# Kernel tuning notes

Hardware: AMD Instinct MI355X
Metric: run time of the kernel (lower is better)

## Reference

```python
import jax, jax.numpy as jnp
import numpy as np

B, S, HID = 1, 2048, 2048
NUM_HEADS, NUM_KV_HEADS, HEAD_DIM = 16, 4, 128
ROPE_THETA = 10000.0
EPS = 1e-6


def setup_inputs() -> dict:
    key = jax.random.key(0)
    ks = jax.random.split(key, 9)
    s = 0.02
    return {
        "hidden_states": jax.random.normal(ks[0], (B, S, HID), jnp.float32),
        "mu_prev": jax.random.normal(ks[1], (B, S, HID), jnp.float32),
        "wq": jax.random.normal(ks[2], (NUM_HEADS * HEAD_DIM, HID), jnp.float32) * s,
        "wk": jax.random.normal(ks[3], (NUM_KV_HEADS * HEAD_DIM, HID), jnp.float32) * s,
        "wv": jax.random.normal(ks[4], (NUM_KV_HEADS * HEAD_DIM, HID), jnp.float32) * s,
        "wo": jax.random.normal(ks[5], (HID, NUM_HEADS * HEAD_DIM), jnp.float32) * s,
        "wmq": jax.random.normal(ks[6], (NUM_HEADS * HEAD_DIM, HID), jnp.float32) * (s * 0.1),
        "wmk": jax.random.normal(ks[7], (NUM_KV_HEADS * HEAD_DIM, HID), jnp.float32) * (s * 0.1),
        "wmv": jax.random.normal(ks[8], (NUM_KV_HEADS * HEAD_DIM, HID), jnp.float32) * (s * 0.1),
        "q_norm_w": jnp.ones((HEAD_DIM,), jnp.float32),
        "k_norm_w": jnp.ones((HEAD_DIM,), jnp.float32),
    }


def _rmsnorm(x, w):
    var = jnp.mean(jnp.square(x), axis=-1, keepdims=True)
    return x * jax.lax.rsqrt(var + EPS) * w


def _rope_cos_sin(seq_len, dtype):
    inv_freq = 1.0 / (ROPE_THETA ** (jnp.arange(0, HEAD_DIM, 2, dtype=jnp.float32) / HEAD_DIM))
    freqs = jnp.arange(seq_len, dtype=jnp.float32)[:, None] * inv_freq[None, :]  # [S, D/2]
    emb = jnp.concatenate([freqs, freqs], axis=-1)  # [S, D]
    return jnp.cos(emb).astype(dtype), jnp.sin(emb).astype(dtype)


def _rotate_half(x):
    x1, x2 = jnp.split(x, 2, axis=-1)
    return jnp.concatenate([-x2, x1], axis=-1)


def reference(hidden_states, mu_prev, wq, wk, wv, wo, wmq, wmk, wmv, q_norm_w, k_norm_w):
    b, s, _ = hidden_states.shape
    # Fused mu-guided QKV projections (cat(x, mu) @ cat(W, Wm)^T == x@W^T + mu@Wm^T)
    q = hidden_states @ wq.T + mu_prev @ wmq.T  # [B,S,H*D]
    k = hidden_states @ wk.T + mu_prev @ wmk.T  # [B,S,KV*D]
    v = hidden_states @ wv.T + mu_prev @ wmv.T
    q = q.reshape(b, s, NUM_HEADS, HEAD_DIM).transpose(0, 2, 1, 3)      # [B,H,S,D]
    k = k.reshape(b, s, NUM_KV_HEADS, HEAD_DIM).transpose(0, 2, 1, 3)   # [B,KV,S,D]
    v = v.reshape(b, s, NUM_KV_HEADS, HEAD_DIM).transpose(0, 2, 1, 3)
    # per-head QK RMSNorm
    q = _rmsnorm(q, q_norm_w)
    k = _rmsnorm(k, k_norm_w)
    # RoPE
    cos, sin = _rope_cos_sin(s, q.dtype)
    q = q * cos + _rotate_half(q) * sin
    k = k * cos + _rotate_half(k) * sin
    # GQA attention without materializing repeated K/V: group query heads
    g = NUM_HEADS // NUM_KV_HEADS
    qg = q.reshape(b, NUM_KV_HEADS, g, s, HEAD_DIM)
    scale = 1.0 / jnp.sqrt(jnp.asarray(HEAD_DIM, q.dtype))
    scores = jnp.einsum('bkgqd,bkld->bkgql', qg, k) * scale  # [B,KV,G,S,S]
    causal = jnp.tril(jnp.ones((s, s), bool))
    scores = jnp.where(causal, scores, jnp.asarray(-jnp.inf, scores.dtype))
    probs = jax.nn.softmax(scores.astype(jnp.float32), axis=-1).astype(q.dtype)
    out = jnp.einsum('bkgql,bkld->bkgqd', probs, v)  # [B,KV,G,S,D]
    out = out.reshape(b, NUM_HEADS, s, HEAD_DIM).transpose(0, 2, 1, 3).reshape(b, s, NUM_HEADS * HEAD_DIM)
    return out @ wo.T
```

## Files before the change

kernel.cpp:

```cpp
#include <hip/hip_runtime.h>
#include <math.h>

#define SEQ 2048
#define HID_DIM 2048
#define NH 16
#define NKV 4
#define HD 128
#define QS 3072

typedef float  f4v  __attribute__((ext_vector_type(4)));
typedef __bf16 bf8v __attribute__((ext_vector_type(8)));
typedef __bf16 bf4v __attribute__((ext_vector_type(4)));
typedef __bf16 bf2v __attribute__((ext_vector_type(2)));

typedef __attribute__((address_space(1))) const void* gvp;
typedef __attribute__((address_space(3))) void*       svp;

__device__ __forceinline__ void gld16(const void* g, void* lds_wave_base) {
    __builtin_amdgcn_global_load_lds((gvp)g, (svp)lds_wave_base, 16, 0, 0);
}

__device__ __forceinline__ void wgb() {
    asm volatile("" ::: "memory");
    __builtin_amdgcn_s_barrier();
    asm volatile("" ::: "memory");
}
#define VMC(n) asm volatile("s_waitcnt vmcnt(" #n ")" ::: "memory")

__global__ __launch_bounds__(256)
void cvt_all(__bf16* __restrict__ Acat, __bf16* __restrict__ Wcat,
             __bf16* __restrict__ Wo,
             const float* __restrict__ hs, const float* __restrict__ mu,
             const float* __restrict__ wq, const float* __restrict__ wmq,
             const float* __restrict__ wk, const float* __restrict__ wmk,
             const float* __restrict__ wv, const float* __restrict__ wmv,
             const float* __restrict__ wo)
{
    int b = blockIdx.x;
    const float *s0, *s1; __bf16* dst;
    if (b < 8192)       { s0 = hs; s1 = mu;  dst = Acat; }
    else if (b < 16384) { s0 = wq; s1 = wmq; dst = Wcat;                            b -= 8192; }
    else if (b < 18432) { s0 = wk; s1 = wmk; dst = Wcat + (size_t)2048 * 4096;      b -= 16384; }
    else if (b < 20480) { s0 = wv; s1 = wmv; dst = Wcat + (size_t)2560 * 4096;      b -= 18432; }
    else {
        int i = (b - 20480) * 256 + threadIdx.x;
        float4 v = *reinterpret_cast<const float4*>(wo + (size_t)i * 4);
        *reinterpret_cast<bf4v*>(Wo + (size_t)i * 4) =
            bf4v{ (__bf16)v.x, (__bf16)v.y, (__bf16)v.z, (__bf16)v.w };
        return;
    }
    int i = b * 256 + threadIdx.x;
    int row = i >> 10, c = i & 1023;
    const float* s = (c < 512) ? s0 + ((size_t)row * 512 + c) * 4
                               : s1 + ((size_t)row * 512 + (c - 512)) * 4;
    float4 v = *reinterpret_cast<const float4*>(s);
    *reinterpret_cast<bf4v*>(dst + ((size_t)row * 1024 + c) * 4) =
        bf4v{ (__bf16)v.x, (__bf16)v.y, (__bf16)v.z, (__bf16)v.w };
}

__device__ __forceinline__ void stage_half(
    const __bf16* __restrict__ g, int ldk, int row0, int ktile, int half,
    char* buf, int w, int sr, int sc)
{
#pragma unroll
    for (int j = 0; j < 2; ++j) {
        int sid = w * 2 + j;
        int rb = half * 8 + (sid >> 1), cb = sid & 1;
        gld16(g + (size_t)(row0 + rb * 16 + sr) * ldk + ktile * 64 + cb * 32 + sc,
              buf + (rb * 2 + cb) * 1024);
    }
}
__device__ __forceinline__ void stage_tile(
    const __bf16* __restrict__ g, int ldk, int row0, int ktile,
    char* buf, int w, int sr, int sc)
{
    stage_half(g, ldk, row0, ktile, 0, buf, w, sr, sc);
    stage_half(g, ldk, row0, ktile, 1, buf, w, sr, sc);
}

#define LOAD_AF(DST, BUF, MTB) \
    _Pragma("unroll") for (int mt = 0; mt < 4; ++mt) \
    _Pragma("unroll") for (int ks = 0; ks < 2; ++ks) \
        DST[mt][ks] = *(const bf8v*)((BUF) + (((wm * 8 + (MTB) + mt) * 2 + ks) << 10) + frag_off);
#define LOAD_BF(DST, BUF, NTB) \
    _Pragma("unroll") for (int nt = 0; nt < 2; ++nt) \
    _Pragma("unroll") for (int ks = 0; ks < 2; ++ks) \
        DST[nt][ks] = *(const bf8v*)((BUF) + (((wn * 4 + (NTB) + nt) * 2 + ks) << 10) + frag_off);
#define MFMA_Q(MTB, NTB, AR, BR) \
    __builtin_amdgcn_s_setprio(1); \
    _Pragma("unroll") for (int mt = 0; mt < 4; ++mt) \
    _Pragma("unroll") for (int nt = 0; nt < 2; ++nt) \
    _Pragma("unroll") for (int ks = 0; ks < 2; ++ks) \
        acc[(MTB) + mt][(NTB) + nt] = __builtin_amdgcn_mfma_f32_16x16x32_bf16( \
            AR[mt][ks], BR[nt][ks], acc[(MTB) + mt][(NTB) + nt], 0, 0, 0); \
    __builtin_amdgcn_s_setprio(0);

__global__ __launch_bounds__(512, 2)
void gemm_nt_pl(const __bf16* __restrict__ A, const __bf16* __restrict__ B,
                __bf16* __restrict__ P, int M, int N, int K, int KS)
{
    __shared__ __align__(1024) char lds[131072];
    char* A0 = lds;
    char* A1 = lds + 32768;
    char* B0 = lds + 65536;
    char* B1 = lds + 98304;

    const int tid = threadIdx.x, lane = tid & 63, w = tid >> 6;
    const int wm = w >> 2, wn = w & 3;
    const int mm = lane & 15, quad = lane >> 4;
    const int m0 = blockIdx.y * 256, n0 = blockIdx.x * 256;
    const int kt0 = (blockIdx.z * KS) >> 6;
    const int T = KS >> 6;

    const int sr = lane >> 2, sc = (lane & 3) * 8;
    const int frag_off = (mm * 4 + quad) << 4;

    f4v acc[8][4] = {};
    bf8v aLo[4][2], aHi[4][2], b01e[2][2], b01o[2][2], b23[2][2];

    stage_tile(A, K, m0, kt0,     A0, w, sr, sc);
    stage_tile(B, K, n0, kt0,     B0, w, sr, sc);
    stage_tile(A, K, m0, kt0 + 1, A1, w, sr, sc);
    stage_tile(B, K, n0, kt0 + 1, B1, w, sr, sc);
    VMC(8);
    wgb();
    LOAD_AF(aLo, A0, 0)
    LOAD_BF(b01e, B0, 0)

    const int nbody = (T - 2) >> 1;
    for (int it = 0; it < nbody; ++it) {
        const int t2 = kt0 + 2 * it + 2, t3 = t2 + 1;
        LOAD_BF(b23, B0, 2)
        MFMA_Q(0, 0, aLo, b01e)
        wgb();
        LOAD_AF(aHi, A0, 4)
        MFMA_Q(0, 2, aLo, b23)
        VMC(0);
        wgb();
        LOAD_AF(aLo, A1, 0)
        stage_tile(B, K, n0, t2, B0, w, sr, sc);
        MFMA_Q(4, 2, aHi, b23)
        wgb();
        LOAD_BF(b01o, B1, 0)
        stage_tile(A, K, m0, t2, A0, w, sr, sc);
        MFMA_Q(4, 0, aHi, b01e)
        wgb();
        LOAD_BF(b23, B1, 2)
        MFMA_Q(0, 0, aLo, b01o)
        wgb();
        LOAD_AF(aHi, A1, 4)
        MFMA_Q(0, 2, aLo, b23)
        VMC(0);
        wgb();
        LOAD_AF(aLo, A0, 0)
        stage_tile(B, K, n0, t3, B1, w, sr, sc);
        MFMA_Q(4, 2, aHi, b23)
        wgb();
        LOAD_BF(b01e, B0, 0)
        stage_tile(A, K, m0, t3, A1, w, sr, sc);
        MFMA_Q(4, 0, aHi, b01o)
        wgb();
    }
    LOAD_BF(b23, B0, 2)
    MFMA_Q(0, 0, aLo, b01e)
    wgb();
    LOAD_AF(aHi, A0, 4)
    MFMA_Q(0, 2, aLo, b23)
    VMC(0);
    wgb();
    LOAD_AF(aLo, A1, 0)
    MFMA_Q(4, 2, aHi, b23)
    wgb();
    LOAD_BF(b01o, B1, 0)
    MFMA_Q(4, 0, aHi, b01e)
    wgb();
    LOAD_BF(b23, B1, 2)
    MFMA_Q(0, 0, aLo, b01o)
    wgb();
    LOAD_AF(aHi, A1, 4)
    MFMA_Q(0, 2, aLo, b23)
    wgb();
    MFMA_Q(4, 2, aHi, b23)
    MFMA_Q(4, 0, aHi, b01o)

    __bf16* Pz = P + (size_t)blockIdx.z * M * N;
#pragma unroll
    for (int mt = 0; mt < 8; ++mt)
#pragma unroll
        for (int nt = 0; nt < 4; ++nt)
#pragma unroll
            for (int r = 0; r < 4; ++r)
                Pz[(size_t)(m0 + wm * 128 + mt * 16 + quad * 4 + r) * N
                   + n0 + wn * 64 + nt * 16 + mm] = (__bf16)acc[mt][nt][r];
}

__global__ __launch_bounds__(256)
void add4(const __bf16* __restrict__ P, float* __restrict__ out, int n4)
{
    int i = blockIdx.x * 256 + threadIdx.x;
    if (i >= n4) return;
    float4 s = {0.f, 0.f, 0.f, 0.f};
#pragma unroll
    for (int z = 0; z < 4; ++z) {
        bf4v v = *reinterpret_cast<const bf4v*>(P + (size_t)z * n4 * 4 + (size_t)i * 4);
        s.x += (float)v[0]; s.y += (float)v[1]; s.z += (float)v[2]; s.w += (float)v[3];
    }
    *reinterpret_cast<float4*>(out + (size_t)i * 4) = s;
}

__global__ __launch_bounds__(256)
void norm_rope_pk(__bf16* __restrict__ qkv ,
                  const __bf16* __restrict__ p1,
                  const float* __restrict__ qw, const float* __restrict__ kw,
                  __bf16* __restrict__ Kt)
{
    const int s = blockIdx.x, hh = blockIdx.y * 4 + threadIdx.y, l = threadIdx.x;
    const float* wn; float scale; int off;
    if (hh < NH) { off = hh * HD;               wn = qw; scale = 0.08838834764831845f; }
    else         { off = 2048 + (hh - NH) * HD; wn = kw; scale = 1.0f; }
    __bf16* p = qkv + (size_t)s * QS + off;
    const __bf16* q1 = p1 + (size_t)s * QS + off;
    float x0 = (float)p[l]      + (float)q1[l];
    float x1 = (float)p[l + 64] + (float)q1[l + 64];
    float ss = x0 * x0 + x1 * x1;
#pragma unroll
    for (int o = 32; o; o >>= 1) ss += __shfl_xor(ss, o);
    float inv = rsqrtf(ss * (1.0f / 128.0f) + 1e-6f);
    x0 *= inv * wn[l];
    x1 *= inv * wn[l + 64];
    float invf = exp2f(-(float)l * (13.287712379549449f / 64.0f));
    float ang  = (float)s * invf;
    float c, sn;
    sincosf(ang, &sn, &c);
    float y0 = (x0 * c - x1 * sn) * scale;
    float y1 = (x1 * c + x0 * sn) * scale;
    if (hh < NH) {
        p[l]      = (__bf16)y0;
        p[l + 64] = (__bf16)y1;
    } else {
        const int kh = hh - NH, key = s & 63;
        char* tile = (char*)Kt + (size_t)(kh * 32 + (s >> 6)) * 16384 + key * 256;
        const int sw = (key & 15) << 4;
        *reinterpret_cast<__bf16*>(tile + ((((l)      >> 3) << 4) ^ sw) + (l & 7) * 2)        = (__bf16)y0;
        *reinterpret_cast<__bf16*>(tile + ((((l + 64) >> 3) << 4) ^ sw) + (l & 7) * 2)        = (__bf16)y1;
    }
}

__global__ __launch_bounds__(256)
void pack_v(const __bf16* __restrict__ qkv0, const __bf16* __restrict__ qkv1,
            __bf16* __restrict__ Vt)
{
    const int kt = blockIdx.x, kh = blockIdx.y, t = threadIdx.x;
    char* tile = (char*)Vt + ((size_t)(kh * 32 + kt)) * 16384;
    const __bf16* s0 = qkv0 + 2560 + kh * HD;
    const __bf16* s1 = qkv1 + 2560 + kh * HD;
#pragma unroll
    for (int i = 0; i < 4; ++i) {
        int cid = t * 4 + i;
        int d = cid >> 3, kcp = cid & 7;
        int kc = kcp ^ (d & 7);
        size_t base = (size_t)(kt * 64 + kc * 8) * QS + d;
        __bf16 tmp[8];
#pragma unroll
        for (int j = 0; j < 8; ++j)
            tmp[j] = (__bf16)((float)s0[base + (size_t)j * QS] +
                              (float)s1[base + (size_t)j * QS]);
        *reinterpret_cast<bf8v*>(tile + cid * 16) = *reinterpret_cast<bf8v*>(tmp);
    }
}

__global__ __launch_bounds__(512)
void attn_split(const __bf16* __restrict__ qkv,
                const __bf16* __restrict__ Kt, const __bf16* __restrict__ Vt,
                __bf16* __restrict__ Op, float* __restrict__ Lp)
{
    __shared__ char Ks[32768];
    __shared__ char Vs[32768];
    __shared__ char Ps[8][2048];

    const int c = blockIdx.x, qt = 15 - blockIdx.y, h = blockIdx.z;
    if (c * 8 > qt) return;
    const int kend = min(qt, c * 8 + 7);
    const int tid = threadIdx.x, lane = tid & 63, w = tid >> 6;
    const int mm = lane & 15, quad = lane >> 4;
    const int kh = h >> 2;

    bf8v aq[4];
    const __bf16* qbase = qkv + (size_t)(qt * 128 + w * 16 + mm) * QS + h * HD;
#pragma unroll
    for (int ks = 0; ks < 4; ++ks)
        aq[ks] = *reinterpret_cast<const bf8v*>(qbase + ks * 32 + quad * 8);

    float lp[4] = {};
    f4v oacc[8] = {};

    const char* kbase = (const char*)Kt + (size_t)(kh * 32) * 16384;
    const char* vbase = (const char*)Vt + (size_t)(kh * 32) * 16384;

    for (int tt = c * 8; tt <= kend; ++tt) {
        wgb();
#pragma unroll
        for (int j = 0; j < 4; ++j) {
            int chunk = w * 4 + j;
            gld16(kbase + (size_t)tt * 32768 + chunk * 1024 + lane * 16,
                  Ks + chunk * 1024);
            gld16(vbase + (size_t)tt * 32768 + chunk * 1024 + lane * 16,
                  Vs + chunk * 1024);
        }
        VMC(0);
        wgb();

        const int nss = (tt == qt && w < 4) ? 1 : 2;
        for (int ss = 0; ss < nss; ++ss) {
            const char* Ksub = Ks + ss * 16384;
            const char* Vsub = Vs + ss * 16384;

            f4v s[4] = {};
#pragma unroll
            for (int ks = 0; ks < 4; ++ks)
#pragma unroll
                for (int c16 = 0; c16 < 4; ++c16) {
                    bf8v b = *reinterpret_cast<const bf8v*>(
                        Ksub + (c16 * 16 + mm) * 256 + (((ks * 4 + quad) ^ mm) << 4));
                    s[c16] = __builtin_amdgcn_mfma_f32_16x16x32_bf16(aq[ks], b, s[c16], 0, 0, 0);
                }
            if (tt == qt) {
#pragma unroll
                for (int c16 = 0; c16 < 4; ++c16)
#pragma unroll
                    for (int r = 0; r < 4; ++r)
                        if (ss * 64 + c16 * 16 + mm > w * 16 + quad * 4 + r)
                            s[c16][r] = -__builtin_inff();
            }
            float pr[4][4];
#pragma unroll
            for (int c16 = 0; c16 < 4; ++c16)
#pragma unroll
                for (int r = 0; r < 4; ++r) {
                    pr[c16][r] = __expf(s[c16][r]);
                    lp[r] += pr[c16][r];
                }
#pragma unroll
            for (int c16 = 0; c16 < 4; ++c16)
#pragma unroll
                for (int r = 0; r < 4; ++r) {
                    float mine  = pr[c16][r];
                    float other = __shfl_xor(mine, 1);
                    if ((mm & 1) == 0) {
                        int roww = quad * 4 + r;
                        int cc   = c16 * 2 + (mm >> 3);
                        *reinterpret_cast<bf2v*>(
                            &Ps[w][roww * 128 + ((cc ^ (roww & 7)) << 4) + (mm & 7) * 2]) =
                            bf2v{ (__bf16)mine, (__bf16)other };
                    }
                }
            bf8v pa[2];
#pragma unroll
            for (int kb = 0; kb < 2; ++kb)
                pa[kb] = *reinterpret_cast<const bf8v*>(
                    &Ps[w][mm * 128 + (((kb * 4 + quad) ^ (mm & 7)) << 4)]);
#pragma unroll
            for (int nb = 0; nb < 8; ++nb) {
                int d = nb * 16 + mm;
#pragma unroll
                for (int kb = 0; kb < 2; ++kb) {
                    bf8v bv = *reinterpret_cast<const bf8v*>(
                        Vsub + d * 128 + (((kb * 4 + quad) ^ (d & 7)) << 4));
                    oacc[nb] = __builtin_amdgcn_mfma_f32_16x16x32_bf16(pa[kb], bv, oacc[nb], 0, 0, 0);
                }
            }
        }
    }
#pragma unroll
    for (int off = 1; off < 16; off <<= 1)
#pragma unroll
        for (int r = 0; r < 4; ++r) lp[r] += __shfl_xor(lp[r], off);
#pragma unroll
    for (int r = 0; r < 4; ++r) {
        int row = qt * 128 + w * 16 + quad * 4 + r;
        size_t obase = ((size_t)(c * 16 + h) * SEQ + row) * HD;
#pragma unroll
        for (int nb = 0; nb < 8; ++nb)
            Op[obase + nb * 16 + mm] = (__bf16)oacc[nb][r];
        if (mm == 0)
            Lp[(size_t)(c * 16 + h) * SEQ + row] = lp[r];
    }
}

__global__ __launch_bounds__(256)
void combine(const __bf16* __restrict__ Op, const float* __restrict__ Lp,
             __bf16* __restrict__ ab)
{
    const int row = blockIdx.x, h = blockIdx.y * 4 + threadIdx.y, l = threadIdx.x;
    const int nch = (row >> 10) + 1;
    float L = 0.f, a0 = 0.f, a1 = 0.f;
    for (int c = 0; c < nch; ++c) {
        L += Lp[(size_t)(c * 16 + h) * SEQ + row];
        bf2v p = *reinterpret_cast<const bf2v*>(
            Op + ((size_t)(c * 16 + h) * SEQ + row) * HD + 2 * l);
        a0 += (float)p[0];
        a1 += (float)p[1];
    }
    float inv = 1.f / L;
    *reinterpret_cast<bf2v*>(ab + (size_t)row * (NH * HD) + h * HD + 2 * l) =
        bf2v{ (__bf16)(a0 * inv), (__bf16)(a1 * inv) };
}

extern "C" void kernel_launch(void* const* d_in, const int* in_sizes, int n_in,
                              void* d_out, int out_size, void* d_ws, size_t ws_size,
                              hipStream_t stream)
{
    const float* hs  = (const float*)d_in[0];
    const float* mu  = (const float*)d_in[1];
    const float* wq  = (const float*)d_in[2];
    const float* wk  = (const float*)d_in[3];
    const float* wv  = (const float*)d_in[4];
    const float* wo  = (const float*)d_in[5];
    const float* wmq = (const float*)d_in[6];
    const float* wmk = (const float*)d_in[7];
    const float* wmv = (const float*)d_in[8];
    const float* qw  = (const float*)d_in[9];
    const float* kw  = (const float*)d_in[10];
    float* out = (float*)d_out;

    char* ws = (char*)d_ws;
    __bf16* Wcat = (__bf16*)(ws + 0);
    __bf16* Acat = (__bf16*)(ws + 25165824);
    __bf16* Wo   = (__bf16*)(ws + 41943040);
    __bf16* qkvp = (__bf16*)(ws + 50331648);
    __bf16* ab   = (__bf16*)(ws + 75497472);
    __bf16* Ktl  = (__bf16*)(ws + 0);
    __bf16* Vtl  = (__bf16*)(ws + 2097152);
    __bf16* Opart= (__bf16*)(ws + 4194304);
    float*  Lpart= (float*) (ws + 37748736);
    __bf16* outp = (__bf16*)(ws + 0);

    cvt_all<<<dim3(24576), 256, 0, stream>>>(Acat, Wcat, Wo,
                                             hs, mu, wq, wmq, wk, wmk, wv, wmv, wo);

    gemm_nt_pl<<<dim3(QS / 256, SEQ / 256, 2), 512, 0, stream>>>(Acat, Wcat, qkvp, SEQ, QS, 2 * HID_DIM, HID_DIM);
    norm_rope_pk<<<dim3(SEQ, 5), dim3(64, 4), 0, stream>>>(qkvp, qkvp + (size_t)SEQ * QS, qw, kw, Ktl);
    pack_v<<<dim3(32, NKV), 256, 0, stream>>>(qkvp, qkvp + (size_t)SEQ * QS, Vtl);
    attn_split<<<dim3(2, 16, NH), 512, 0, stream>>>(qkvp, Ktl, Vtl, Opart, Lpart);
    combine<<<dim3(SEQ, 4), dim3(64, 4), 0, stream>>>(Opart, Lpart, ab);
    gemm_nt_pl<<<dim3(HID_DIM / 256, SEQ / 256, 4), 512, 0, stream>>>(ab, Wo, outp, SEQ, HID_DIM, NH * HD, 512);
    add4<<<dim3((1024 * 1024 + 255) / 256), 256, 0, stream>>>(outp, out, 1024 * 1024);
}
```

Baseline: 317.9 us.

## Fuse V packing into norm kernel, atomic split-K output, XCD-aware block remap

Drops the separate pack_v kernel by giving norm_rope_pk a sixth grid row that sums the two split-K partials for V and scatters them into the swizzled V tile layout. The output projection now accumulates its split-K partials with fp32 atomicAdd into a zeroed output, which removes the bf16 partial buffer and the add4 reduction kernel. Both the GEMM and the attention kernels remap flat block indices so that consecutive blocks are spread across the 8 XCDs. This costs a memset plus atomic contention, and the summation order becomes nondeterministic.

Result: slower. 352.8 us (+11.0%).

```diff
diff --git a/kernel.cpp b/kernel.cpp
--- a/kernel.cpp
+++ b/kernel.cpp
@@ -97,7 +97,8 @@
 
 __global__ __launch_bounds__(512, 2)
 void gemm_nt_pl(const __bf16* __restrict__ A, const __bf16* __restrict__ B,
-                __bf16* __restrict__ P, int M, int N, int K, int KS)
+                __bf16* __restrict__ P, int M, int N, int K, int KS,
+                float* __restrict__ OutF, int mode)
 {
     __shared__ __align__(1024) char lds[131072];
     char* A0 = lds;
@@ -108,8 +109,15 @@
     const int tid = threadIdx.x, lane = tid & 63, w = tid >> 6;
     const int wm = w >> 2, wn = w & 3;
     const int mm = lane & 15, quad = lane >> 4;
-    const int m0 = blockIdx.y * 256, n0 = blockIdx.x * 256;
-    const int kt0 = (blockIdx.z * KS) >> 6;
+
+    const int nbx = gridDim.x, nby = gridDim.y;
+    int flat = blockIdx.x + nbx * (blockIdx.y + nby * blockIdx.z);
+    const int cpx = (nbx * nby * gridDim.z) >> 3;
+    flat = (flat & 7) * cpx + (flat >> 3);
+    const int bxi = flat % nbx, byi = (flat / nbx) % nby, bzi = flat / (nbx * nby);
+
+    const int m0 = byi * 256, n0 = bxi * 256;
+    const int kt0 = (bzi * KS) >> 6;
     const int T = KS >> 6;
 
     const int sr = lane >> 2, sc = (lane & 3) * 8;
@@ -183,38 +191,49 @@
     MFMA_Q(4, 2, aHi, b23)
     MFMA_Q(4, 0, aHi, b01o)
 
-    __bf16* Pz = P + (size_t)blockIdx.z * M * N;
-#pragma unroll
-    for (int mt = 0; mt < 8; ++mt)
-#pragma unroll
-        for (int nt = 0; nt < 4; ++nt)
-#pragma unroll
-            for (int r = 0; r < 4; ++r)
-                Pz[(size_t)(m0 + wm * 128 + mt * 16 + quad * 4 + r) * N
-                   + n0 + wn * 64 + nt * 16 + mm] = (__bf16)acc[mt][nt][r];
-}
-
-__global__ __launch_bounds__(256)
-void add4(const __bf16* __restrict__ P, float* __restrict__ out, int n4)
-{
-    int i = blockIdx.x * 256 + threadIdx.x;
-    if (i >= n4) return;
-    float4 s = {0.f, 0.f, 0.f, 0.f};
-#pragma unroll
-    for (int z = 0; z < 4; ++z) {
-        bf4v v = *reinterpret_cast<const bf4v*>(P + (size_t)z * n4 * 4 + (size_t)i * 4);
-        s.x += (float)v[0]; s.y += (float)v[1]; s.z += (float)v[2]; s.w += (float)v[3];
-    }
-    *reinterpret_cast<float4*>(out + (size_t)i * 4) = s;
+    if (mode) {
+#pragma unroll
+        for (int mt = 0; mt < 8; ++mt)
+#pragma unroll
+            for (int nt = 0; nt < 4; ++nt)
+#pragma unroll
+                for (int r = 0; r < 4; ++r)
+                    atomicAdd(&OutF[(size_t)(m0 + wm * 128 + mt * 16 + quad * 4 + r) * N
+                                    + n0 + wn * 64 + nt * 16 + mm], acc[mt][nt][r]);
+    } else {
+        __bf16* Pz = P + (size_t)bzi * M * N;
+#pragma unroll
+        for (int mt = 0; mt < 8; ++mt)
+#pragma unroll
+            for (int nt = 0; nt < 4; ++nt)
+#pragma unroll
+                for (int r = 0; r < 4; ++r)
+                    Pz[(size_t)(m0 + wm * 128 + mt * 16 + quad * 4 + r) * N
+                       + n0 + wn * 64 + nt * 16 + mm] = (__bf16)acc[mt][nt][r];
+    }
 }
 
 __global__ __launch_bounds__(256)
 void norm_rope_pk(__bf16* __restrict__ qkv ,
                   const __bf16* __restrict__ p1,
                   const float* __restrict__ qw, const float* __restrict__ kw,
-                  __bf16* __restrict__ Kt)
+                  __bf16* __restrict__ Kt, __bf16* __restrict__ Vt)
 {
     const int s = blockIdx.x, hh = blockIdx.y * 4 + threadIdx.y, l = threadIdx.x;
+    if (hh >= NH + NKV) {
+        const int vh = hh - (NH + NKV);
+        const int off = 2560 + vh * HD;
+        const __bf16* p  = qkv + (size_t)s * QS + off;
+        const __bf16* q1 = p1  + (size_t)s * QS + off;
+        float x0 = (float)p[l]      + (float)q1[l];
+        float x1 = (float)p[l + 64] + (float)q1[l + 64];
+        char* tile = (char*)Vt + (size_t)(vh * 32 + (s >> 6)) * 16384;
+        const int kc = (s >> 3) & 7, j = s & 7;
+        const int d2 = l + 64;
+        *reinterpret_cast<__bf16*>(tile + l  * 128 + ((kc ^ (l  & 7)) << 4) + j * 2) = (__bf16)x0;
+        *reinterpret_cast<__bf16*>(tile + d2 * 128 + ((kc ^ (d2 & 7)) << 4) + j * 2) = (__bf16)x1;
+        return;
+    }
     const float* wn; float scale; int off;
     if (hh < NH) { off = hh * HD;               wn = qw; scale = 0.08838834764831845f; }
     else         { off = 2048 + (hh - NH) * HD; wn = kw; scale = 1.0f; }
@@ -241,31 +260,8 @@
         const int kh = hh - NH, key = s & 63;
         char* tile = (char*)Kt + (size_t)(kh * 32 + (s >> 6)) * 16384 + key * 256;
         const int sw = (key & 15) << 4;
-        *reinterpret_cast<__bf16*>(tile + ((((l)      >> 3) << 4) ^ sw) + (l & 7) * 2)        = (__bf16)y0;
-        *reinterpret_cast<__bf16*>(tile + ((((l + 64) >> 3) << 4) ^ sw) + (l & 7) * 2)        = (__bf16)y1;
-    }
-}
-
-__global__ __launch_bounds__(256)
-void pack_v(const __bf16* __restrict__ qkv0, const __bf16* __restrict__ qkv1,
-            __bf16* __restrict__ Vt)
-{
-    const int kt = blockIdx.x, kh = blockIdx.y, t = threadIdx.x;
-    char* tile = (char*)Vt + ((size_t)(kh * 32 + kt)) * 16384;
-    const __bf16* s0 = qkv0 + 2560 + kh * HD;
-    const __bf16* s1 = qkv1 + 2560 + kh * HD;
-#pragma unroll
-    for (int i = 0; i < 4; ++i) {
-        int cid = t * 4 + i;
-        int d = cid >> 3, kcp = cid & 7;
-        int kc = kcp ^ (d & 7);
-        size_t base = (size_t)(kt * 64 + kc * 8) * QS + d;
-        __bf16 tmp[8];
-#pragma unroll
-        for (int j = 0; j < 8; ++j)
-            tmp[j] = (__bf16)((float)s0[base + (size_t)j * QS] +
-                              (float)s1[base + (size_t)j * QS]);
-        *reinterpret_cast<bf8v*>(tile + cid * 16) = *reinterpret_cast<bf8v*>(tmp);
+        *reinterpret_cast<__bf16*>(tile + ((((l)      >> 3) << 4) ^ sw) + (l & 7) * 2) = (__bf16)y0;
+        *reinterpret_cast<__bf16*>(tile + ((((l + 64) >> 3) << 4) ^ sw) + (l & 7) * 2) = (__bf16)y1;
     }
 }
 
@@ -278,7 +274,10 @@
     __shared__ char Vs[32768];
     __shared__ char Ps[8][2048];
 
-    const int c = blockIdx.x, qt = 15 - blockIdx.y, h = blockIdx.z;
+    int flat = blockIdx.x + 2 * (blockIdx.y + 16 * blockIdx.z);
+    flat = (flat & 7) * 64 + (flat >> 3);
+    const int c = flat & 1, qt = 15 - ((flat >> 1) & 15), h = flat >> 5;
+
     if (c * 8 > qt) return;
     const int kend = min(qt, c * 8 + 7);
     const int tid = threadIdx.x, lane = tid & 63, w = tid >> 6;
@@ -433,16 +432,17 @@
     __bf16* Vtl  = (__bf16*)(ws + 2097152);
     __bf16* Opart= (__bf16*)(ws + 4194304);
     float*  Lpart= (float*) (ws + 37748736);
-    __bf16* outp = (__bf16*)(ws + 0);
 
     cvt_all<<<dim3(24576), 256, 0, stream>>>(Acat, Wcat, Wo,
                                              hs, mu, wq, wmq, wk, wmk, wv, wmv, wo);
 
-    gemm_nt_pl<<<dim3(QS / 256, SEQ / 256, 2), 512, 0, stream>>>(Acat, Wcat, qkvp, SEQ, QS, 2 * HID_DIM, HID_DIM);
-    norm_rope_pk<<<dim3(SEQ, 5), dim3(64, 4), 0, stream>>>(qkvp, qkvp + (size_t)SEQ * QS, qw, kw, Ktl);
-    pack_v<<<dim3(32, NKV), 256, 0, stream>>>(qkvp, qkvp + (size_t)SEQ * QS, Vtl);
+    gemm_nt_pl<<<dim3(QS / 256, SEQ / 256, 2), 512, 0, stream>>>(
+        Acat, Wcat, qkvp, SEQ, QS, 2 * HID_DIM, HID_DIM, nullptr, 0);
+    norm_rope_pk<<<dim3(SEQ, 6), dim3(64, 4), 0, stream>>>(
+        qkvp, qkvp + (size_t)SEQ * QS, qw, kw, Ktl, Vtl);
     attn_split<<<dim3(2, 16, NH), 512, 0, stream>>>(qkvp, Ktl, Vtl, Opart, Lpart);
     combine<<<dim3(SEQ, 4), dim3(64, 4), 0, stream>>>(Opart, Lpart, ab);
-    gemm_nt_pl<<<dim3(HID_DIM / 256, SEQ / 256, 4), 512, 0, stream>>>(ab, Wo, outp, SEQ, HID_DIM, NH * HD, 512);
-    add4<<<dim3((1024 * 1024 + 255) / 256), 256, 0, stream>>>(outp, out, 1024 * 1024);
-}
+    hipMemsetAsync(out, 0, (size_t)SEQ * HID_DIM * sizeof(float), stream);
+    gemm_nt_pl<<<dim3(HID_DIM / 256, SEQ / 256, 4), 512, 0, stream>>>(
+        ab, Wo, nullptr, SEQ, HID_DIM, NH * HD, 512, out, 1);
+}
```
